# Kernel tuning notes

Hardware: AMD Instinct MI355X
Metric: run time of the kernel (lower is better)

## Reference

```python
import jax, jax.numpy as jnp
from jax import lax
import numpy as np

CH = 16      # channel_n
HID = 128    # update MLP width


def setup_inputs() -> dict:
    key = jax.random.key(0)
    ks = jax.random.split(key, 7)
    B, H, W = 4, 224, 224
    x = jax.random.uniform(ks[0], (B, CH, H, W), dtype=jnp.float32)
    # perception: Conv2d(16 -> 48, 3x3, pad 1, no bias), OIHW
    w_percep = jax.random.normal(ks[1], (CH * 3, CH, 3, 3), jnp.float32) * 0.05
    # update MLP: 1x1 convs == pointwise linears over channels
    w1 = jax.random.normal(ks[2], (HID, CH * 3), jnp.float32) * 0.05
    b1 = jax.random.normal(ks[3], (HID,), jnp.float32) * 0.01
    w2 = jax.random.normal(ks[4], (HID, HID), jnp.float32) * 0.05
    b2 = jax.random.normal(ks[5], (HID,), jnp.float32) * 0.01
    w3 = jax.random.normal(ks[6], (CH, HID), jnp.float32) * 0.05  # no bias
    return {"x": x, "w_percep": w_percep, "w1": w1, "b1": b1,
            "w2": w2, "b2": b2, "w3": w3, "steps": 40}


def reference(x, w_percep, w1, b1, w2, b2, w3, steps):
    dn = ("NCHW", "OIHW", "NCHW")

    def step(x, _):
        # 3x3 perception conv, same padding  -> [B, 48, H, W]
        p = lax.conv_general_dilated(x, w_percep, (1, 1), "SAME",
                                     dimension_numbers=dn)
        # pointwise conv-MLP (1x1 convs as channel einsums)
        h = jax.nn.relu(jnp.einsum("bchw,oc->bohw", p, w1) + b1[None, :, None, None])
        h = jax.nn.relu(jnp.einsum("bchw,oc->bohw", h, w2) + b2[None, :, None, None])
        dx = jnp.einsum("bchw,oc->bohw", h, w3)
        # residual update + clamp to [0, 1] (eval mode: no fire mask)
        return jnp.clip(x + dx, 0.0, 1.0), None

    x, _ = lax.scan(step, x, None, length=steps)
    return x
```

## Files before the change

### kernel.cpp

```cpp
#include <hip/hip_runtime.h>


typedef __attribute__((ext_vector_type(8))) short short8;
typedef __attribute__((ext_vector_type(4))) float float4v;
typedef __attribute__((ext_vector_type(2))) float float2v;

#define MFMA16(a, b, c) __builtin_amdgcn_mfma_f32_16x16x32_bf16((a), (b), (c), 0, 0, 0)

__device__ __forceinline__ short f2bf(float f) {
  unsigned u = __builtin_bit_cast(unsigned, f);
  return (short)((u + 0x8000u) >> 16);
}

__device__ __forceinline__ unsigned pk2bf(float a, float b) {
#if __has_builtin(__builtin_amdgcn_cvt_pk_bf16_f32)
  typedef __attribute__((ext_vector_type(2))) __bf16 bf2;
  bf2 r = __builtin_amdgcn_cvt_pk_bf16_f32(a, b);
  return __builtin_bit_cast(unsigned, r);
#else
  unsigned ua = __builtin_bit_cast(unsigned, a), ub = __builtin_bit_cast(unsigned, b);
  return ((ua + 0x8000u) >> 16) | (((ub + 0x8000u) >> 16) << 16);
#endif
}

__device__ __forceinline__ void async16(const void* g, void* l) {
  __builtin_amdgcn_global_load_lds((const __attribute__((address_space(1))) void*)g,
                                   (__attribute__((address_space(3))) void*)l,
                                   16, 0, 0);
}

__device__ __forceinline__ void sync_lds() {
  asm volatile("s_waitcnt lgkmcnt(0)\n\ts_barrier" ::: "memory");
}

#define WS_WE    0
#define WS_W2    43008
#define WS_W3    77824
#define WS_B1    82944
#define WS_B2    83456
#define WS_X32A  83968
#define WS_X32B  12929024
#define WS_X16A  25774080
#define WS_X16B  32196608

__global__ void prep_x(const float* __restrict__ x, float* __restrict__ x32,
                       short* __restrict__ x16) {
  int i = blockIdx.x * 256 + threadIdx.x;
  int w = i % 224;
  int h = (i / 224) % 224;
  int c = (i / 50176) & 15;
  int bb = i / 802816;
  float v = x[i];
  int o = ((bb * 224 + h) * 224 + w) * 16 + c;
  x32[o] = v;
  x16[o] = f2bf(v);
}

__global__ void prep_w(const float* __restrict__ wp, const float* __restrict__ w1,
                       const float* __restrict__ b1, const float* __restrict__ w2,
                       const float* __restrict__ b2, const float* __restrict__ w3,
                       short* __restrict__ wE, short* __restrict__ w2t,
                       short* __restrict__ w3t, float* __restrict__ b1p,
                       float* __restrict__ b2p) {
  int i = blockIdx.x * 256 + threadIdx.x;
  if (i < 21504) {
    int o = i / 168, k = i % 168;
    float v = 0.f;
    if (k < 144) {
      int off = k >> 4, c = k & 15;
      for (int c3 = 0; c3 < 48; ++c3)
        v += w1[o * 48 + c3] * wp[c3 * 144 + c * 9 + off];
    }
    wE[i] = f2bf(v);
  } else if (i < 38912) {
    int j = i - 21504;
    int n = j / 136, kk = j % 136;
    float v = 0.f;
    if (kk < 128) { int ch = 16 * (kk & 7) + (kk >> 3); v = w2[n * 128 + ch]; }
    w2t[j] = f2bf(v);
  } else if (i < 41472) {
    int j = i - 38912;
    float v = 0.f;
    if (j < 2176) {
      int n = j / 136, kk = j % 136;
      if (kk < 128) { int ch = 16 * (kk & 7) + (kk >> 3); v = w3[n * 128 + ch]; }
    }
    w3t[j] = f2bf(v);
  } else if (i < 41600) {
    int p = i - 41472;
    b1p[p] = b1[16 * (p & 7) + (p >> 3)];
  } else {
    int p = i - 41600;
    b2p[p] = b2[16 * (p & 7) + (p >> 3)];
  }
}

template <bool LAST>
__global__ __launch_bounds__(512, 4) void ca_step(
    const short* __restrict__ wEg, const short* __restrict__ w2g,
    const short* __restrict__ w3g, const float* __restrict__ b1p,
    const float* __restrict__ b2p, const float* __restrict__ xs32,
    const short* __restrict__ xs16, float* __restrict__ xd32,
    short* __restrict__ xd16, float* __restrict__ dout) {
  __shared__ short sXH[4 * 3616];
  __shared__ short sBUF[2 * 2176];
  __shared__ short sH2[2 * 2176];

  const int tid = threadIdx.x;
  const int lane = tid & 63;
  const int wv = tid >> 6;
  const int c16 = lane & 15;
  const int q = lane >> 4;
  const int q8 = q * 8;
  const int qh = q >> 1;
  const int c0 = (q & 1) * 8;

  const int blk = blockIdx.x;
  const int b = blk / 112;
  const int h0 = (blk % 112) * 2;

  const short8 z8 = {0, 0, 0, 0, 0, 0, 0, 0};
  for (int t = wv; t < 28; t += 8) {
    int hr = t / 7, ck = t % 7;
    int hh = h0 - 1 + hr;
    char* l = (char*)sXH + hr * 7232 + 32 + ck * 1024;
    if (hh >= 0 && hh < 224) {
      const char* g = (const char*)xs16 + ((size_t)(b * 224 + hh) * 224) * 32 + ck * 1024;
      async16(g + lane * 16, l);
    } else {
      *(short8*)(l + lane * 16) = z8;
    }
  }
  if (tid < 16) {
    int hr = tid >> 2, wch = tid & 3;
    int colb = (wch < 2) ? 0 : 225;
    *(short8*)((char*)sXH + hr * 7232 + colb * 32 + (wch & 1) * 16) = z8;
  }

  if (wv < 4) {
    const int wq = wv;
    short8 wf[5][2];
#pragma unroll
    for (int kc = 0; kc < 5; ++kc)
#pragma unroll
      for (int n = 0; n < 2; ++n)
        wf[kc][n] = *(const short8*)(wEg + ((2 * wq + n) * 16 + c16) * 168 + kc * 32 + q8);
    const float2v bH = *(const float2v*)(b1p + c16 * 8 + 2 * wq);

    __syncthreads();

    for (int j = 0; j < 30; ++j) {
      if (j < 28) {
        const int hb = ((j / 14) * 226 + (j % 14) * 16) * 16;
        float4v acc[2];
        acc[0] = (float4v){0.f, 0.f, 0.f, 0.f};
        acc[1] = (float4v){0.f, 0.f, 0.f, 0.f};
#pragma unroll
        for (int kc = 0; kc < 5; ++kc) {
          int off = kc * 2 + qh;
          if (off > 8) off = 8;
          int dy = (off * 11) >> 5;
          int dxx = off - dy * 3;
          short8 a = *(const short8*)(sXH + hb + (dy * 226 + dxx + c16) * 16 + c0);
          acc[0] = MFMA16(a, wf[kc][0], acc[0]);
          acc[1] = MFMA16(a, wf[kc][1], acc[1]);
        }
        short* dst = sBUF + (j & 1) * 2176;
#pragma unroll
        for (int r = 0; r < 4; ++r) {
          unsigned d = pk2bf(fmaxf(acc[0][r] + bH[0], 0.f),
                             fmaxf(acc[1][r] + bH[1], 0.f));
          *(unsigned*)(dst + (q * 4 + r) * 136 + c16 * 8 + 2 * wq) = d;
        }
      }
      sync_lds();
    }
  } else {
    const int g = wv - 4;
    short8 w2f[4][2];
    short8 w3f[4];
#pragma unroll
    for (int kc = 0; kc < 4; ++kc)
#pragma unroll
      for (int n = 0; n < 2; ++n)
        w2f[kc][n] = *(const short8*)(w2g + ((2 * g + n) * 16 + c16) * 136 + kc * 32 + q8);
#pragma unroll
    for (int kc = 0; kc < 4; ++kc)
      w3f[kc] = *(const short8*)(w3g + c16 * 136 + kc * 32 + q8);
    const float2v bG = *(const float2v*)(b2p + c16 * 8 + 2 * g);

    __syncthreads();

    for (int j = 0; j < 30; ++j) {
      const bool own3 = (j >= 2) && (((j - 2) & 3) == g);
      float xres[4];
      int cb3 = 0, hglob3 = 0;
      if (own3) {
        const int t3 = j - 2;
        cb3 = (t3 % 14) * 16; hglob3 = h0 + t3 / 14;
#pragma unroll
        for (int r = 0; r < 4; ++r) {
          size_t pix = (size_t)(b * 224 + hglob3) * 224 + cb3 + q * 4 + r;
          xres[r] = xs32[pix * 16 + c16];
        }
      }
      if (j >= 1 && j <= 28) {
        const short* src = sBUF + ((j - 1) & 1) * 2176;
        float4v acc2[2];
        acc2[0] = (float4v){0.f, 0.f, 0.f, 0.f};
        acc2[1] = (float4v){0.f, 0.f, 0.f, 0.f};
#pragma unroll
        for (int kc = 0; kc < 4; ++kc) {
          short8 a = *(const short8*)(src + c16 * 136 + kc * 32 + q8);
          acc2[0] = MFMA16(a, w2f[kc][0], acc2[0]);
          acc2[1] = MFMA16(a, w2f[kc][1], acc2[1]);
        }
        short* dsth2 = sH2 + (j & 1) * 2176;
#pragma unroll
        for (int r = 0; r < 4; ++r) {
          unsigned d = pk2bf(fmaxf(acc2[0][r] + bG[0], 0.f),
                             fmaxf(acc2[1][r] + bG[1], 0.f));
          *(unsigned*)(dsth2 + (q * 4 + r) * 136 + c16 * 8 + 2 * g) = d;
        }
      }
      if (own3) {
        const short* srch2 = sH2 + ((j - 1) & 1) * 2176;
        float4v acc3 = (float4v){0.f, 0.f, 0.f, 0.f};
#pragma unroll
        for (int kc = 0; kc < 4; ++kc) {
          short8 a = *(const short8*)(srch2 + c16 * 136 + kc * 32 + q8);
          acc3 = MFMA16(a, w3f[kc], acc3);
        }
#pragma unroll
        for (int r = 0; r < 4; ++r) {
          int col = cb3 + q * 4 + r;
          size_t pix = (size_t)(b * 224 + hglob3) * 224 + col;
          float v = xres[r] + acc3[r];
          v = fminf(fmaxf(v, 0.f), 1.f);
          if (LAST) {
            dout[((size_t)(b * 16 + c16) * 224 + hglob3) * 224 + col] = v;
          } else {
            xd32[pix * 16 + c16] = v;
            xd16[pix * 16 + c16] = f2bf(v);
          }
        }
      }
      sync_lds();
    }
  }
}

extern "C" void kernel_launch(void* const* d_in, const int* in_sizes, int n_in,
                              void* d_out, int out_size, void* d_ws, size_t ws_size,
                              hipStream_t stream) {
  const float* x  = (const float*)d_in[0];
  const float* wp = (const float*)d_in[1];
  const float* w1 = (const float*)d_in[2];
  const float* b1 = (const float*)d_in[3];
  const float* w2 = (const float*)d_in[4];
  const float* b2 = (const float*)d_in[5];
  const float* w3 = (const float*)d_in[6];

  char* ws = (char*)d_ws;
  short* wEg = (short*)(ws + WS_WE);
  short* w2g = (short*)(ws + WS_W2);
  short* w3g = (short*)(ws + WS_W3);
  float* b1p = (float*)(ws + WS_B1);
  float* b2p = (float*)(ws + WS_B2);
  float* X32[2] = {(float*)(ws + WS_X32A), (float*)(ws + WS_X32B)};
  short* X16[2] = {(short*)(ws + WS_X16A), (short*)(ws + WS_X16B)};

  prep_x<<<12544, 256, 0, stream>>>(x, X32[0], X16[0]);
  prep_w<<<163, 256, 0, stream>>>(wp, w1, b1, w2, b2, w3, wEg, w2g, w3g, b1p, b2p);

  for (int s = 0; s < 39; ++s) {
    int sb = s & 1;
    ca_step<false><<<448, 512, 0, stream>>>(wEg, w2g, w3g, b1p, b2p,
                                            X32[sb], X16[sb],
                                            X32[1 - sb], X16[1 - sb], nullptr);
  }
  ca_step<true><<<448, 512, 0, stream>>>(wEg, w2g, w3g, b1p, b2p,
                                         X32[1], X16[1],
                                         X32[0], X16[0], (float*)d_out);
}
```

Measured before the change: 1.185 ms.

## Switch CA step to 32x32 MFMA tiles with weights-as-A and 32-pixel chunks

Recasts the perception and hidden-layer GEMMs to use 32x32x16 bf16 MFMA with weights as the A operand and 32-pixel tiles, halving the pipeline iterations per block from 30 to 16 and cutting the number of barriers. Weight layouts become plain row-major (no padded/interleaved prep), biases and w3 are staged into LDS, and the final layer is done by two waves with vectorized float4 residual loads and stores. It trades more LDS and accumulator registers (16-wide accumulators) for fewer instructions and syncs, and leaves the output-layer work on only half the waves.

```diff
diff --git a/kernel.cpp b/kernel.cpp
--- a/kernel.cpp
+++ b/kernel.cpp
@@ -3,8 +3,10 @@
 
 typedef __attribute__((ext_vector_type(8))) short short8;
 typedef __attribute__((ext_vector_type(4))) float float4v;
-typedef __attribute__((ext_vector_type(2))) float float2v;
-
+typedef __attribute__((ext_vector_type(16))) float float16v;
+typedef __attribute__((ext_vector_type(2))) unsigned uint2v;
+
+#define MFMA32(a, b, c) __builtin_amdgcn_mfma_f32_32x32x16_bf16((a), (b), (c), 0, 0, 0)
 #define MFMA16(a, b, c) __builtin_amdgcn_mfma_f32_16x16x32_bf16((a), (b), (c), 0, 0, 0)
 
 __device__ __forceinline__ short f2bf(float f) {
@@ -34,14 +36,12 @@
 }
 
 #define WS_WE    0
-#define WS_W2    43008
-#define WS_W3    77824
-#define WS_B1    82944
-#define WS_B2    83456
-#define WS_X32A  83968
-#define WS_X32B  12929024
-#define WS_X16A  25774080
-#define WS_X16B  32196608
+#define WS_W2    36864
+#define WS_W3    69632
+#define WS_X32A  73728
+#define WS_X32B  12918784
+#define WS_X16A  25763840
+#define WS_X16B  32186368
 
 __global__ void prep_x(const float* __restrict__ x, float* __restrict__ x32,
                        short* __restrict__ x16) {
@@ -57,63 +57,45 @@
 }
 
 __global__ void prep_w(const float* __restrict__ wp, const float* __restrict__ w1,
-                       const float* __restrict__ b1, const float* __restrict__ w2,
-                       const float* __restrict__ b2, const float* __restrict__ w3,
+                       const float* __restrict__ w2, const float* __restrict__ w3,
                        short* __restrict__ wE, short* __restrict__ w2t,
-                       short* __restrict__ w3t, float* __restrict__ b1p,
-                       float* __restrict__ b2p) {
+                       short* __restrict__ w3t) {
   int i = blockIdx.x * 256 + threadIdx.x;
-  if (i < 21504) {
-    int o = i / 168, k = i % 168;
+  if (i < 18432) {
+    int o = i / 144, k = i % 144;
+    int off = k >> 4, c = k & 15;
     float v = 0.f;
-    if (k < 144) {
-      int off = k >> 4, c = k & 15;
-      for (int c3 = 0; c3 < 48; ++c3)
-        v += w1[o * 48 + c3] * wp[c3 * 144 + c * 9 + off];
-    }
+    for (int c3 = 0; c3 < 48; ++c3)
+      v += w1[o * 48 + c3] * wp[c3 * 144 + c * 9 + off];
     wE[i] = f2bf(v);
-  } else if (i < 38912) {
-    int j = i - 21504;
-    int n = j / 136, kk = j % 136;
-    float v = 0.f;
-    if (kk < 128) { int ch = 16 * (kk & 7) + (kk >> 3); v = w2[n * 128 + ch]; }
-    w2t[j] = f2bf(v);
-  } else if (i < 41472) {
-    int j = i - 38912;
-    float v = 0.f;
-    if (j < 2176) {
-      int n = j / 136, kk = j % 136;
-      if (kk < 128) { int ch = 16 * (kk & 7) + (kk >> 3); v = w3[n * 128 + ch]; }
-    }
-    w3t[j] = f2bf(v);
-  } else if (i < 41600) {
-    int p = i - 41472;
-    b1p[p] = b1[16 * (p & 7) + (p >> 3)];
+  } else if (i < 34816) {
+    int j = i - 18432;
+    w2t[j] = f2bf(w2[j]);
   } else {
-    int p = i - 41600;
-    b2p[p] = b2[16 * (p & 7) + (p >> 3)];
+    int j = i - 34816;
+    w3t[j] = f2bf(w3[j]);
   }
 }
 
 template <bool LAST>
 __global__ __launch_bounds__(512, 4) void ca_step(
     const short* __restrict__ wEg, const short* __restrict__ w2g,
-    const short* __restrict__ w3g, const float* __restrict__ b1p,
-    const float* __restrict__ b2p, const float* __restrict__ xs32,
+    const short* __restrict__ w3g, const float* __restrict__ b1,
+    const float* __restrict__ b2, const float* __restrict__ xs32,
     const short* __restrict__ xs16, float* __restrict__ xd32,
     short* __restrict__ xd16, float* __restrict__ dout) {
   __shared__ short sXH[4 * 3616];
-  __shared__ short sBUF[2 * 2176];
-  __shared__ short sH2[2 * 2176];
+  __shared__ short sBUF[2 * 4352];
+  __shared__ short sH2[2 * 4352];
+  __shared__ short sW3[2048];
+  __shared__ float sB1[128];
+  __shared__ float sB2[128];
 
   const int tid = threadIdx.x;
   const int lane = tid & 63;
   const int wv = tid >> 6;
-  const int c16 = lane & 15;
-  const int q = lane >> 4;
-  const int q8 = q * 8;
-  const int qh = q >> 1;
-  const int c0 = (q & 1) * 8;
+  const int nn = lane & 31;
+  const int kh = lane >> 5;
 
   const int blk = blockIdx.x;
   const int b = blk / 112;
@@ -136,113 +118,116 @@
     int colb = (wch < 2) ? 0 : 225;
     *(short8*)((char*)sXH + hr * 7232 + colb * 32 + (wch & 1) * 16) = z8;
   }
+  if (tid < 128) sB1[tid] = b1[tid];
+  else if (tid < 256) sB2[tid - 128] = b2[tid - 128];
+  for (int i = tid; i < 2048; i += 512) sW3[i] = w3g[i];
 
   if (wv < 4) {
     const int wq = wv;
-    short8 wf[5][2];
-#pragma unroll
-    for (int kc = 0; kc < 5; ++kc)
-#pragma unroll
-      for (int n = 0; n < 2; ++n)
-        wf[kc][n] = *(const short8*)(wEg + ((2 * wq + n) * 16 + c16) * 168 + kc * 32 + q8);
-    const float2v bH = *(const float2v*)(b1p + c16 * 8 + 2 * wq);
+    short8 wf[9];
+#pragma unroll
+    for (int o = 0; o < 9; ++o)
+      wf[o] = *(const short8*)(wEg + (32 * wq + nn) * 144 + o * 16 + 8 * kh);
 
     __syncthreads();
 
-    for (int j = 0; j < 30; ++j) {
-      if (j < 28) {
-        const int hb = ((j / 14) * 226 + (j % 14) * 16) * 16;
-        float4v acc[2];
-        acc[0] = (float4v){0.f, 0.f, 0.f, 0.f};
-        acc[1] = (float4v){0.f, 0.f, 0.f, 0.f};
-#pragma unroll
-        for (int kc = 0; kc < 5; ++kc) {
-          int off = kc * 2 + qh;
-          if (off > 8) off = 8;
-          int dy = (off * 11) >> 5;
-          int dxx = off - dy * 3;
-          short8 a = *(const short8*)(sXH + hb + (dy * 226 + dxx + c16) * 16 + c0);
-          acc[0] = MFMA16(a, wf[kc][0], acc[0]);
-          acc[1] = MFMA16(a, wf[kc][1], acc[1]);
-        }
-        short* dst = sBUF + (j & 1) * 2176;
-#pragma unroll
-        for (int r = 0; r < 4; ++r) {
-          unsigned d = pk2bf(fmaxf(acc[0][r] + bH[0], 0.f),
-                             fmaxf(acc[1][r] + bH[1], 0.f));
-          *(unsigned*)(dst + (q * 4 + r) * 136 + c16 * 8 + 2 * wq) = d;
+    for (int j = 0; j < 16; ++j) {
+      if (j < 14) {
+        const int rr = (2 * j) / 14;
+        const int pb = ((2 * j) % 14) * 16;
+        float16v acc;
+#pragma unroll
+        for (int i = 0; i < 16; ++i) acc[i] = 0.f;
+        const int abase = ((rr)*226 + pb + nn) * 16 + 8 * kh;
+#pragma unroll 3
+        for (int o = 0; o < 9; ++o) {
+          int dy = (o * 11) >> 5;
+          int dx = o - dy * 3;
+          short8 bf = *(const short8*)(sXH + abase + (dy * 226 + dx) * 16);
+          acc = MFMA32(wf[o], bf, acc);
+        }
+        short* dst = sBUF + (j & 1) * 4352 + nn * 136 + 32 * wq + 4 * kh;
+#pragma unroll
+        for (int G = 0; G < 4; ++G) {
+          float4v bv = *(const float4v*)(sB1 + 32 * wq + 8 * G + 4 * kh);
+          uint2v pk;
+          pk[0] = pk2bf(fmaxf(acc[4 * G + 0] + bv[0], 0.f),
+                        fmaxf(acc[4 * G + 1] + bv[1], 0.f));
+          pk[1] = pk2bf(fmaxf(acc[4 * G + 2] + bv[2], 0.f),
+                        fmaxf(acc[4 * G + 3] + bv[3], 0.f));
+          *(uint2v*)(dst + 8 * G) = pk;
         }
       }
       sync_lds();
     }
   } else {
     const int g = wv - 4;
-    short8 w2f[4][2];
-    short8 w3f[4];
-#pragma unroll
-    for (int kc = 0; kc < 4; ++kc)
-#pragma unroll
-      for (int n = 0; n < 2; ++n)
-        w2f[kc][n] = *(const short8*)(w2g + ((2 * g + n) * 16 + c16) * 136 + kc * 32 + q8);
-#pragma unroll
-    for (int kc = 0; kc < 4; ++kc)
-      w3f[kc] = *(const short8*)(w3g + c16 * 136 + kc * 32 + q8);
-    const float2v bG = *(const float2v*)(b2p + c16 * 8 + 2 * g);
+    const int c16 = lane & 15;
+    const int q = lane >> 4;
+    short8 w2f[8];
+#pragma unroll
+    for (int u = 0; u < 8; ++u)
+      w2f[u] = *(const short8*)(w2g + (32 * g + nn) * 128 + u * 16 + 8 * kh);
 
     __syncthreads();
 
-    for (int j = 0; j < 30; ++j) {
-      const bool own3 = (j >= 2) && (((j - 2) & 3) == g);
-      float xres[4];
-      int cb3 = 0, hglob3 = 0;
-      if (own3) {
-        const int t3 = j - 2;
-        cb3 = (t3 % 14) * 16; hglob3 = h0 + t3 / 14;
-#pragma unroll
-        for (int r = 0; r < 4; ++r) {
-          size_t pix = (size_t)(b * 224 + hglob3) * 224 + cb3 + q * 4 + r;
-          xres[r] = xs32[pix * 16 + c16];
-        }
-      }
-      if (j >= 1 && j <= 28) {
-        const short* src = sBUF + ((j - 1) & 1) * 2176;
-        float4v acc2[2];
-        acc2[0] = (float4v){0.f, 0.f, 0.f, 0.f};
-        acc2[1] = (float4v){0.f, 0.f, 0.f, 0.f};
+    for (int j = 0; j < 16; ++j) {
+      float4v xres;
+      size_t pixg = 0;
+      int rr3 = 0, pb3 = 0;
+      if (g < 2 && j >= 2) {
+        rr3 = (2 * (j - 2)) / 14;
+        pb3 = ((2 * (j - 2)) % 14) * 16;
+        pixg = (size_t)(b * 224 + h0 + rr3) * 224 + pb3 + 16 * g + c16;
+        xres = *(const float4v*)(xs32 + pixg * 16 + 4 * q);
+      }
+      if (j >= 1 && j <= 14) {
+        const short* src = sBUF + ((j - 1) & 1) * 4352 + nn * 136 + 8 * kh;
+        float16v acc2;
+#pragma unroll
+        for (int i = 0; i < 16; ++i) acc2[i] = 0.f;
+#pragma unroll 2
+        for (int u = 0; u < 8; ++u) {
+          short8 bf = *(const short8*)(src + u * 16);
+          acc2 = MFMA32(w2f[u], bf, acc2);
+        }
+        short* dst = sH2 + (j & 1) * 4352 + nn * 136 + 32 * g + 4 * kh;
+#pragma unroll
+        for (int G = 0; G < 4; ++G) {
+          float4v bv = *(const float4v*)(sB2 + 32 * g + 8 * G + 4 * kh);
+          uint2v pk;
+          pk[0] = pk2bf(fmaxf(acc2[4 * G + 0] + bv[0], 0.f),
+                        fmaxf(acc2[4 * G + 1] + bv[1], 0.f));
+          pk[1] = pk2bf(fmaxf(acc2[4 * G + 2] + bv[2], 0.f),
+                        fmaxf(acc2[4 * G + 3] + bv[3], 0.f));
+          *(uint2v*)(dst + 8 * G) = pk;
+        }
+      }
+      if (g < 2 && j >= 2) {
+        const short* sh = sH2 + ((j - 1) & 1) * 4352 + (16 * g + c16) * 136;
+        float4v acc3 = (float4v){0.f, 0.f, 0.f, 0.f};
 #pragma unroll
         for (int kc = 0; kc < 4; ++kc) {
-          short8 a = *(const short8*)(src + c16 * 136 + kc * 32 + q8);
-          acc2[0] = MFMA16(a, w2f[kc][0], acc2[0]);
-          acc2[1] = MFMA16(a, w2f[kc][1], acc2[1]);
-        }
-        short* dsth2 = sH2 + (j & 1) * 2176;
-#pragma unroll
-        for (int r = 0; r < 4; ++r) {
-          unsigned d = pk2bf(fmaxf(acc2[0][r] + bG[0], 0.f),
-                             fmaxf(acc2[1][r] + bG[1], 0.f));
-          *(unsigned*)(dsth2 + (q * 4 + r) * 136 + c16 * 8 + 2 * g) = d;
-        }
-      }
-      if (own3) {
-        const short* srch2 = sH2 + ((j - 1) & 1) * 2176;
-        float4v acc3 = (float4v){0.f, 0.f, 0.f, 0.f};
-#pragma unroll
-        for (int kc = 0; kc < 4; ++kc) {
-          short8 a = *(const short8*)(srch2 + c16 * 136 + kc * 32 + q8);
-          acc3 = MFMA16(a, w3f[kc], acc3);
-        }
-#pragma unroll
-        for (int r = 0; r < 4; ++r) {
-          int col = cb3 + q * 4 + r;
-          size_t pix = (size_t)(b * 224 + hglob3) * 224 + col;
-          float v = xres[r] + acc3[r];
-          v = fminf(fmaxf(v, 0.f), 1.f);
-          if (LAST) {
-            dout[((size_t)(b * 16 + c16) * 224 + hglob3) * 224 + col] = v;
-          } else {
-            xd32[pix * 16 + c16] = v;
-            xd16[pix * 16 + c16] = f2bf(v);
-          }
+          short8 af = *(const short8*)(sW3 + c16 * 128 + kc * 32 + q * 8);
+          short8 bf = *(const short8*)(sh + kc * 32 + q * 8);
+          acc3 = MFMA16(af, bf, acc3);
+        }
+        float vo[4];
+#pragma unroll
+        for (int r = 0; r < 4; ++r)
+          vo[r] = fminf(fmaxf(xres[r] + acc3[r], 0.f), 1.f);
+        if (LAST) {
+#pragma unroll
+          for (int r = 0; r < 4; ++r)
+            dout[((size_t)(b * 16 + 4 * q + r) * 224 + h0 + rr3) * 224 +
+                 pb3 + 16 * g + c16] = vo[r];
+        } else {
+          *(float4v*)(xd32 + pixg * 16 + 4 * q) =
+              (float4v){vo[0], vo[1], vo[2], vo[3]};
+          uint2v p16;
+          p16[0] = pk2bf(vo[0], vo[1]);
+          p16[1] = pk2bf(vo[2], vo[3]);
+          *(uint2v*)(xd16 + pixg * 16 + 4 * q) = p16;
         }
       }
       sync_lds();
@@ -265,21 +250,19 @@
   short* wEg = (short*)(ws + WS_WE);
   short* w2g = (short*)(ws + WS_W2);
   short* w3g = (short*)(ws + WS_W3);
-  float* b1p = (float*)(ws + WS_B1);
-  float* b2p = (float*)(ws + WS_B2);
   float* X32[2] = {(float*)(ws + WS_X32A), (float*)(ws + WS_X32B)};
   short* X16[2] = {(short*)(ws + WS_X16A), (short*)(ws + WS_X16B)};
 
   prep_x<<<12544, 256, 0, stream>>>(x, X32[0], X16[0]);
-  prep_w<<<163, 256, 0, stream>>>(wp, w1, b1, w2, b2, w3, wEg, w2g, w3g, b1p, b2p);
+  prep_w<<<144, 256, 0, stream>>>(wp, w1, w2, w3, wEg, w2g, w3g);
 
   for (int s = 0; s < 39; ++s) {
     int sb = s & 1;
-    ca_step<false><<<448, 512, 0, stream>>>(wEg, w2g, w3g, b1p, b2p,
+    ca_step<false><<<448, 512, 0, stream>>>(wEg, w2g, w3g, b1, b2,
                                             X32[sb], X16[sb],
                                             X32[1 - sb], X16[1 - sb], nullptr);
   }
-  ca_step<true><<<448, 512, 0, stream>>>(wEg, w2g, w3g, b1p, b2p,
+  ca_step<true><<<448, 512, 0, stream>>>(wEg, w2g, w3g, b1, b2,
                                          X32[1], X16[1],
                                          X32[0], X16[0], (float*)d_out);
 }
```

After: 2.966 ms. +150.2%, slower.
